# Performance work log

Hardware: AMD Instinct MI355X
Metric: run time of the kernel (lower is better)

Reference implementation:

```python
import jax, jax.numpy as jnp
import numpy as np

D_MODEL = 1024
B, S = 4, 4096


def setup_inputs() -> dict:
    key = jax.random.key(0)
    k1, k2, k3, k4, k5 = jax.random.split(key, 5)
    lim = 1.0 / np.sqrt(D_MODEL)  # nn.Linear default init range
    x = jax.random.normal(k1, (B, S, D_MODEL), dtype=jnp.float32)
    mask = jnp.ones((B, S), dtype=jnp.float32)
    W_up = jax.random.uniform(k2, (D_MODEL, D_MODEL), jnp.float32, -lim, lim)
    b_up = jax.random.uniform(k3, (D_MODEL,), jnp.float32, -lim, lim)
    W_f = jax.random.uniform(k4, (D_MODEL, D_MODEL), jnp.float32, -lim, lim)
    b_f = jax.random.uniform(k5, (D_MODEL,), jnp.float32, -lim, lim)
    decay_param = jnp.zeros((1,), dtype=jnp.float32)
    return {"x": x, "mask": mask, "W_up": W_up, "b_up": b_up,
            "W_f": W_f, "b_f": b_f, "decay_param": decay_param}


def _decay_scan(u, decay):
    # h_t = decay * h_{t-1} + u_t  along axis=1, via associative scan.
    # Element: (a, b) representing h -> a*h + b; compose: (a1*a2, b1*a2 + b2).
    a = jnp.broadcast_to(decay, u.shape)

    def combine(c1, c2):
        a1, b1 = c1
        a2, b2 = c2
        return a1 * a2, b1 * a2 + b2

    _, h = jax.lax.associative_scan(combine, (a, u), axis=1)
    return h


def reference(x, mask, W_up, b_up, W_f, b_f, decay_param):
    decay = jax.nn.sigmoid(decay_param)[0]
    # u_i = mask_i * linear_update(x_i)
    u = (jnp.einsum('bsd,ed->bse', x, W_up) + b_up) * mask[..., None]
    # h_t = sum_{i<=t} decay^(t-i) * u_i  (exponential-decay recurrence)
    h = _decay_scan(u, decay)
    return jnp.einsum('bsd,ed->bse', h, W_f) + b_f
```

## Files before the change

kernel.cpp:

```cpp
#include <hip/hip_runtime.h>
#include <hip/hip_bf16.h>
#include <cstdint>
#include <cstddef>

#define DMODEL 1024
#define BATCH  4
#define SEQ    4096
#define BSROWS (BATCH*SEQ)
#define CHUNK  32
#define NCHUNK (SEQ/CHUNK)
#define NCH_T  (BATCH*NCHUNK)

typedef __attribute__((ext_vector_type(8))) short bf16x8;
typedef __attribute__((ext_vector_type(4))) float f32x4;


__device__ __forceinline__ unsigned short f2bf(float f) {
  union { float f; uint32_t u; } v; v.f = f;
  uint32_t u = v.u;
  u += 0x7FFFu + ((u >> 16) & 1u);
  return (unsigned short)(u >> 16);
}

__device__ __forceinline__ float sigmoid_dev(const float* dp) {
  return 1.0f / (1.0f + expf(-dp[0]));
}

typedef __attribute__((address_space(1))) void void_g;
typedef __attribute__((address_space(3))) void void_l;

__device__ __forceinline__ void gl2lds16(const void* g, void* l) {
  __builtin_amdgcn_global_load_lds((void_g*)g, (void_l*)l, 16, 0, 0);
}

__device__ __forceinline__ void kloop64(
    const unsigned short* __restrict__ A, const unsigned short* __restrict__ B,
    int m0, int n0, f32x4 acc[2][2],
    unsigned short* As, unsigned short* Bs, int tid) {
  int lane = tid & 63, w = tid >> 6, wm = w & 1, wn = w >> 1;
  int quad = lane >> 4, l16 = lane & 15;
  int r = tid >> 3, cch = tid & 7;
  int g = cch ^ (r & 7);

  auto stage = [&](int t, int slot) {
    int k0 = t * 64;
    unsigned short* dA = As + slot * 4096;
    unsigned short* dB = Bs + slot * 4096;
    gl2lds16(A + (size_t)(m0 + r) * DMODEL + k0 + g * 8,      dA + r * 64 + cch * 8);
    gl2lds16(A + (size_t)(m0 + 32 + r) * DMODEL + k0 + g * 8, dA + (32 + r) * 64 + cch * 8);
    gl2lds16(B + (size_t)(n0 + r) * DMODEL + k0 + g * 8,      dB + r * 64 + cch * 8);
    gl2lds16(B + (size_t)(n0 + 32 + r) * DMODEL + k0 + g * 8, dB + (32 + r) * 64 + cch * 8);
  };
  auto compute = [&](int slot) {
    const bf16x8* Av = (const bf16x8*)(As + slot * 4096);
    const bf16x8* Bv = (const bf16x8*)(Bs + slot * 4096);
    #pragma unroll
    for (int kk = 0; kk < 2; ++kk) {
      bf16x8 af[2], bfr[2];
      #pragma unroll
      for (int i = 0; i < 2; ++i) {
        int rowA = wm * 32 + i * 16 + l16;
        af[i]  = Av[rowA * 8 + ((kk * 4 + quad) ^ (l16 & 7))];
        int rowB = wn * 32 + i * 16 + l16;
        bfr[i] = Bv[rowB * 8 + ((kk * 4 + quad) ^ (l16 & 7))];
      }
      __builtin_amdgcn_s_setprio(1);
      #pragma unroll
      for (int i = 0; i < 2; ++i)
        #pragma unroll
        for (int j = 0; j < 2; ++j)
          acc[i][j] = __builtin_amdgcn_mfma_f32_16x16x32_bf16(af[i], bfr[j], acc[i][j], 0, 0, 0);
      __builtin_amdgcn_s_setprio(0);
    }
  };

  stage(0, 0); stage(1, 1);
  asm volatile("s_waitcnt vmcnt(4)" ::: "memory");
  __builtin_amdgcn_s_barrier();
  asm volatile("" ::: "memory");
  int cur = 0;
  for (int t = 0; t < 14; ++t) {
    int ns = cur + 2; if (ns >= 3) ns -= 3;
    stage(t + 2, ns);
    compute(cur);
    asm volatile("s_waitcnt vmcnt(4)" ::: "memory");
    __builtin_amdgcn_s_barrier();
    asm volatile("" ::: "memory");
    cur = (cur == 2) ? 0 : cur + 1;
  }
  compute(cur);
  asm volatile("s_waitcnt vmcnt(0)" ::: "memory");
  __builtin_amdgcn_s_barrier();
  asm volatile("" ::: "memory");
  cur = (cur == 2) ? 0 : cur + 1;
  compute(cur);
}

__global__ __launch_bounds__(256) void prep_kernel(
    const float* __restrict__ x, const float* __restrict__ mask,
    const float* __restrict__ W_up, const float* __restrict__ b_up,
    const float* __restrict__ W_f, const float* __restrict__ dp,
    unsigned short* __restrict__ Wf_bf, unsigned short* __restrict__ WupT,
    float* __restrict__ bb, unsigned short* __restrict__ hv,
    float* __restrict__ carry, float* __restrict__ lbeta,
    float* __restrict__ cbeta) {
  __shared__ float tile[32][33];
  int blk = blockIdx.x;
  int tid = threadIdx.x;

  if (blk < 512) {
    float decay = sigmoid_dev(dp);
    int b = blk / NCHUNK, c = blk % NCHUNK;
    int base = b * SEQ + c * CHUNK;
    const float4* xp = (const float4*)(x + (size_t)base * DMODEL);
    const float4* mp4 = (const float4*)(mask + base);
    float mreg[32];
    #pragma unroll
    for (int q = 0; q < 8; ++q) {
      float4 t = mp4[q];
      mreg[q * 4 + 0] = t.x; mreg[q * 4 + 1] = t.y;
      mreg[q * 4 + 2] = t.z; mreg[q * 4 + 3] = t.w;
    }
    float4 h = make_float4(0.f, 0.f, 0.f, 0.f);
    #pragma unroll
    for (int s = 0; s < CHUNK; ++s) {
      float m = mreg[s];
      float4 xv = xp[(size_t)s * (DMODEL / 4) + tid];
      h.x = decay * h.x + m * xv.x;
      h.y = decay * h.y + m * xv.y;
      h.z = decay * h.z + m * xv.z;
      h.w = decay * h.w + m * xv.w;
      ushort4 o;
      o.x = f2bf(h.x); o.y = f2bf(h.y); o.z = f2bf(h.z); o.w = f2bf(h.w);
      ((ushort4*)hv)[(size_t)(base + s) * (DMODEL / 4) + tid] = o;
    }
    ((float4*)carry)[(size_t)blk * (DMODEL / 4) + tid] = h;
  } else if (blk < 1536) {
    int e = blk - 512;
    int lane = tid & 63, w = tid >> 6;
    float4 v = ((const float4*)(W_f + (size_t)e * DMODEL))[tid];
    float4 bu = ((const float4*)b_up)[tid];
    ushort4 o;
    o.x = f2bf(v.x); o.y = f2bf(v.y); o.z = f2bf(v.z); o.w = f2bf(v.w);
    ((ushort4*)(Wf_bf + (size_t)e * DMODEL))[tid] = o;
    float s = v.x * bu.x + v.y * bu.y + v.z * bu.z + v.w * bu.w;
    #pragma unroll
    for (int off = 32; off; off >>= 1) s += __shfl_down(s, off);
    if (lane == 0) ((float*)tile)[w] = s;
    __syncthreads();
    if (tid == 0)
      bb[e] = ((float*)tile)[0] + ((float*)tile)[1] +
              ((float*)tile)[2] + ((float*)tile)[3];
  } else if (blk < 2560) {
    int id = blk - 1536;
    int bx = id & 31, by = id >> 5;
    int tx = tid & 31, ty = tid >> 5;
    int xx = bx * 32 + tx;
    int y0 = by * 32;
    for (int j = ty; j < 32; j += 8)
      tile[j][tx] = W_up[(size_t)(y0 + j) * DMODEL + xx];
    __syncthreads();
    int dd = tid >> 3;
    int c4 = (tid & 7) * 4;
    ushort4 o;
    o.x = f2bf(tile[c4 + 0][dd]);
    o.y = f2bf(tile[c4 + 1][dd]);
    o.z = f2bf(tile[c4 + 2][dd]);
    o.w = f2bf(tile[c4 + 3][dd]);
    *(ushort4*)(WupT + (size_t)(bx * 32 + dd) * DMODEL + y0 + c4) = o;
  } else {
    float decay = sigmoid_dev(dp);
    int t = (blk - 2560) * 256 + tid;
    int s = t & 31;
    float h = mask[t];
    float wgt = decay;
    #pragma unroll
    for (int off = 1; off < 32; off <<= 1) {
      float up = __shfl_up(h, off);
      if (s >= off) h += wgt * up;
      wgt = wgt * wgt;
    }
    lbeta[t] = h;
    if (s == 31) cbeta[t >> 5] = h;
  }
}

__global__ __launch_bounds__(256) void mid2_kernel(
    const unsigned short* __restrict__ Wf_bf,
    const unsigned short* __restrict__ WupT,
    unsigned short* __restrict__ Wc,
    const float* __restrict__ carry, const float* __restrict__ cbeta,
    const float* __restrict__ dp,
    unsigned short* __restrict__ Pbf, float* __restrict__ pbeta) {
  __shared__ unsigned short As[3 * 64 * 64];
  __shared__ unsigned short Bs[3 * 64 * 64];
  int tid = threadIdx.x;
  if (blockIdx.x < 256) {
    int mt = blockIdx.x >> 4, nt = blockIdx.x & 15;
    f32x4 acc[2][2] = {};
    kloop64(Wf_bf, WupT, mt * 64, nt * 64, acc, As, Bs, tid);
    int lane = tid & 63, w = tid >> 6, wm = w & 1, wn = w >> 1;
    int quad = lane >> 4, l16 = lane & 15;
    #pragma unroll
    for (int j = 0; j < 2; ++j) {
      int col = nt * 64 + wn * 32 + j * 16 + l16;
      #pragma unroll
      for (int i = 0; i < 2; ++i) {
        int rowb = mt * 64 + wm * 32 + i * 16 + quad * 4;
        #pragma unroll
        for (int rr = 0; rr < 4; ++rr)
          Wc[(size_t)(rowb + rr) * DMODEL + col] = f2bf(acc[i][j][rr]);
      }
    }
  } else {
    float decay = sigmoid_dev(dp);
    float dL = powf(decay, (float)CHUNK);
    int gid = (blockIdx.x - 256) * 256 + tid;
    int b = gid >> 10, dd = gid & 1023;
    float P = 0.f;
    for (int c0 = 0; c0 < NCHUNK; c0 += 8) {
      float v[8];
      #pragma unroll
      for (int j = 0; j < 8; ++j)
        v[j] = carry[(size_t)(b * NCHUNK + c0 + j) * DMODEL + dd];
      #pragma unroll
      for (int j = 0; j < 8; ++j) {
        Pbf[(size_t)(b * NCHUNK + c0 + j) * DMODEL + dd] = f2bf(P);
        P = dL * P + v[j];
      }
    }
    if (dd == 0) {
      float Pb = 0.f;
      for (int c0 = 0; c0 < NCHUNK; c0 += 16) {
        float v[16];
        #pragma unroll
        for (int j = 0; j < 16; ++j) v[j] = cbeta[b * NCHUNK + c0 + j];
        #pragma unroll
        for (int j = 0; j < 16; ++j) {
          pbeta[b * NCHUNK + c0 + j] = Pb;
          Pb = dL * Pb + v[j];
        }
      }
    }
  }
}

__global__ __launch_bounds__(256) void pout_kernel(
    const unsigned short* __restrict__ Pbf,
    const unsigned short* __restrict__ Wc,
    const float* __restrict__ pbeta, const float* __restrict__ bb,
    float* __restrict__ Pout) {
  __shared__ unsigned short As[3 * 64 * 64];
  __shared__ unsigned short Bs[3 * 64 * 64];
  int tid = threadIdx.x;
  int mt = blockIdx.x >> 4, nt = blockIdx.x & 15;
  f32x4 acc[2][2] = {};
  kloop64(Pbf, Wc, mt * 64, nt * 64, acc, As, Bs, tid);
  int lane = tid & 63, w = tid >> 6, wm = w & 1, wn = w >> 1;
  int quad = lane >> 4, l16 = lane & 15;
  #pragma unroll
  for (int j = 0; j < 2; ++j) {
    int col = nt * 64 + wn * 32 + j * 16 + l16;
    float bbv = bb[col];
    #pragma unroll
    for (int i = 0; i < 2; ++i) {
      int rowb = mt * 64 + wm * 32 + i * 16 + quad * 4;
      #pragma unroll
      for (int rr = 0; rr < 4; ++rr) {
        int row = rowb + rr;
        Pout[(size_t)row * DMODEL + col] = acc[i][j][rr] + pbeta[row] * bbv;
      }
    }
  }
}

__global__ __launch_bounds__(512) void gemm_main(
    const unsigned short* __restrict__ A,
    const unsigned short* __restrict__ Bm,
    const float* __restrict__ Pout,
    const float* __restrict__ lbeta,
    const float* __restrict__ bb,
    const float* __restrict__ bias_f,
    const float* __restrict__ dp,
    float* __restrict__ out) {
  __shared__ unsigned short As[4 * 256 * 32];
  __shared__ unsigned short Bs[4 * 256 * 32];
  __shared__ float dpow[CHUNK];
  const int SLOT = 256 * 32;
  int tid = threadIdx.x;
  if (tid < CHUNK) {
    float decay = sigmoid_dev(dp);
    dpow[tid] = powf(decay, (float)(tid + 1));
  }
  __syncthreads();

  int lane = tid & 63, wid = tid >> 6;
  int wm = wid >> 2, wn = wid & 3;
  int quad = lane >> 4, l16 = lane & 15;
  int phi = (l16 >> 1) & 3;
  int r = tid >> 2, c4 = tid & 3;
  int g = c4 ^ ((r >> 1) & 3);

  int bid = blockIdx.x;
  int xcd = bid & 7, jb = bid >> 3;
  int m0 = (xcd * 8 + (jb >> 2)) * 256;
  int n0 = (jb & 3) * 256;

  f32x4 acc[8][4] = {};
  bf16x8 bfr[4];

  auto stageA = [&](int t, int slot) {
    int k0 = t * 32;
    unsigned short* dA = As + slot * SLOT;
    gl2lds16(A + (size_t)(m0 + r) * DMODEL + k0 + g * 8,        dA + r * 32 + c4 * 8);
    gl2lds16(A + (size_t)(m0 + 128 + r) * DMODEL + k0 + g * 8,  dA + (128 + r) * 32 + c4 * 8);
  };
  auto stageB = [&](int t, int slot) {
    int k0 = t * 32;
    unsigned short* dB = Bs + slot * SLOT;
    gl2lds16(Bm + (size_t)(n0 + r) * DMODEL + k0 + g * 8,       dB + r * 32 + c4 * 8);
    gl2lds16(Bm + (size_t)(n0 + 128 + r) * DMODEL + k0 + g * 8, dB + (128 + r) * 32 + c4 * 8);
  };
  auto readA = [&](const bf16x8* Av, int mh, bf16x8 af[4]) {
    #pragma unroll
    for (int i = 0; i < 4; ++i) {
      int rowA = wm * 128 + mh * 64 + i * 16 + l16;
      af[i] = Av[rowA * 4 + (quad ^ phi)];
    }
  };
  auto readB = [&](const bf16x8* Bv) {
    #pragma unroll
    for (int j = 0; j < 4; ++j) {
      int rowB = wn * 64 + j * 16 + l16;
      bfr[j] = Bv[rowB * 4 + (quad ^ phi)];
    }
  };
  auto mfma16 = [&](int mh, const bf16x8 af[4]) {
    __builtin_amdgcn_s_setprio(1);
    #pragma unroll
    for (int i = 0; i < 4; ++i)
      #pragma unroll
      for (int j = 0; j < 4; ++j)
        acc[mh * 4 + i][j] =
            __builtin_amdgcn_mfma_f32_16x16x32_bf16(af[i], bfr[j], acc[mh * 4 + i][j], 0, 0, 0);
    __builtin_amdgcn_s_setprio(0);
  };

  stageA(0, 0); stageB(0, 0);
  stageA(1, 1); stageB(1, 1);
  stageA(2, 2); stageB(2, 2);
  asm volatile("s_waitcnt vmcnt(8)" ::: "memory");
  __builtin_amdgcn_s_barrier();
  asm volatile("" ::: "memory");

  for (int t = 0; t < 29; ++t) {
    int cs = t & 3, ss = (t + 3) & 3;
    const bf16x8* Av = (const bf16x8*)(As + cs * SLOT);
    const bf16x8* Bv = (const bf16x8*)(Bs + cs * SLOT);
    bf16x8 af[4];
    readA(Av, 0, af);
    readB(Bv);
    stageA(t + 3, ss);
    __builtin_amdgcn_s_barrier();
    asm volatile("s_waitcnt lgkmcnt(0)" ::: "memory");
    __builtin_amdgcn_sched_barrier(0);
    mfma16(0, af);
    __builtin_amdgcn_s_barrier();
    bf16x8 af2[4];
    readA(Av, 1, af2);
    stageB(t + 3, ss);
    asm volatile("s_waitcnt vmcnt(8)" ::: "memory");
    __builtin_amdgcn_s_barrier();
    asm volatile("s_waitcnt lgkmcnt(0)" ::: "memory");
    __builtin_amdgcn_sched_barrier(0);
    mfma16(1, af2);
    __builtin_amdgcn_s_barrier();
    asm volatile("" ::: "memory");
  }
  auto tailfull = [&](int slot) {
    const bf16x8* Av = (const bf16x8*)(As + slot * SLOT);
    const bf16x8* Bv = (const bf16x8*)(Bs + slot * SLOT);
    bf16x8 af[4];
    readA(Av, 0, af);
    readB(Bv);
    mfma16(0, af);
    readA(Av, 1, af);
    mfma16(1, af);
  };
  tailfull(1);
  asm volatile("s_waitcnt vmcnt(4)" ::: "memory");
  __builtin_amdgcn_s_barrier();
  asm volatile("" ::: "memory");
  tailfull(2);
  asm volatile("s_waitcnt vmcnt(0)" ::: "memory");
  __builtin_amdgcn_s_barrier();
  asm volatile("" ::: "memory");
  tailfull(3);

  float bbv[4], bfv[4];
  #pragma unroll
  for (int j = 0; j < 4; ++j) {
    int col = n0 + wn * 64 + j * 16 + l16;
    bbv[j] = bb[col];
    bfv[j] = bias_f[col];
  }
  #pragma unroll
  for (int i = 0; i < 8; ++i) {
    #pragma unroll
    for (int rr = 0; rr < 4; ++rr) {
      int row = m0 + wm * 128 + i * 16 + quad * 4 + rr;
      float lb  = lbeta[row];
      float dpw = dpow[row & 31];
      const float* poRow = Pout + (size_t)(row >> 5) * DMODEL;
      float* outRow = out + (size_t)row * DMODEL;
      #pragma unroll
      for (int j = 0; j < 4; ++j) {
        int col = n0 + wn * 64 + j * 16 + l16;
        outRow[col] = acc[i][j][rr] + dpw * poRow[col] + lb * bbv[j] + bfv[j];
      }
    }
  }
}


extern "C" void kernel_launch(void* const* d_in, const int* in_sizes, int n_in,
                              void* d_out, int out_size, void* d_ws, size_t ws_size,
                              hipStream_t stream) {
  const float* x    = (const float*)d_in[0];
  const float* mask = (const float*)d_in[1];
  const float* W_up = (const float*)d_in[2];
  const float* b_up = (const float*)d_in[3];
  const float* W_f  = (const float*)d_in[4];
  const float* b_f  = (const float*)d_in[5];
  const float* dp   = (const float*)d_in[6];
  float* out = (float*)d_out;

  char* ws = (char*)d_ws;
  unsigned short* hv    = (unsigned short*)(ws);
  unsigned short* Wc    = (unsigned short*)(ws + 33554432);
  unsigned short* Wf_bf = (unsigned short*)(ws + 35651584);
  unsigned short* WupT  = (unsigned short*)(ws + 37748736);
  float* carry  = (float*)(ws + 39845888);
  unsigned short* Pbf = (unsigned short*)(ws + 41943040);
  float* Pout   = (float*)(ws + 42991616);
  float* lbeta  = (float*)(ws + 45088768);
  float* cbeta  = (float*)(ws + 45154304);
  float* pbeta  = (float*)(ws + 45156352);
  float* bb     = (float*)(ws + 45158400);

  prep_kernel<<<2624, 256, 0, stream>>>(x, mask, W_up, b_up, W_f, dp,
                                        Wf_bf, WupT, bb, hv, carry, lbeta, cbeta);
  mid2_kernel<<<272, 256, 0, stream>>>(Wf_bf, WupT, Wc, carry, cbeta, dp,
                                       Pbf, pbeta);
  pout_kernel<<<128, 256, 0, stream>>>(Pbf, Wc, pbeta, bb, Pout);
  gemm_main<<<256, 512, 0, stream>>>(hv, Wc, Pout, lbeta, bb, b_f, dp, out);
}
```

Measured before the change: 193.9 us.

## Switch main GEMM to double-buffered K=64 tiles with simpler pipeline

```diff
diff --git a/kernel.cpp b/kernel.cpp
--- a/kernel.cpp
+++ b/kernel.cpp
@@ -283,23 +283,21 @@
     const float* __restrict__ bias_f,
     const float* __restrict__ dp,
     float* __restrict__ out) {
-  __shared__ unsigned short As[4 * 256 * 32];
-  __shared__ unsigned short Bs[4 * 256 * 32];
+  __shared__ unsigned short As[2 * 256 * 64];
+  __shared__ unsigned short Bs[2 * 256 * 64];
   __shared__ float dpow[CHUNK];
-  const int SLOT = 256 * 32;
+  const int TSLOT = 256 * 64;
   int tid = threadIdx.x;
   if (tid < CHUNK) {
     float decay = sigmoid_dev(dp);
     dpow[tid] = powf(decay, (float)(tid + 1));
   }
-  __syncthreads();
 
   int lane = tid & 63, wid = tid >> 6;
   int wm = wid >> 2, wn = wid & 3;
   int quad = lane >> 4, l16 = lane & 15;
-  int phi = (l16 >> 1) & 3;
-  int r = tid >> 2, c4 = tid & 3;
-  int g = c4 ^ ((r >> 1) & 3);
+  int r = tid >> 3, cch = tid & 7;
+  int g = cch ^ (r & 7);
 
   int bid = blockIdx.x;
   int xcd = bid & 7, jb = bid >> 3;
@@ -307,95 +305,56 @@
   int n0 = (jb & 3) * 256;
 
   f32x4 acc[8][4] = {};
-  bf16x8 bfr[4];
-
-  auto stageA = [&](int t, int slot) {
-    int k0 = t * 32;
-    unsigned short* dA = As + slot * SLOT;
-    gl2lds16(A + (size_t)(m0 + r) * DMODEL + k0 + g * 8,        dA + r * 32 + c4 * 8);
-    gl2lds16(A + (size_t)(m0 + 128 + r) * DMODEL + k0 + g * 8,  dA + (128 + r) * 32 + c4 * 8);
+
+  auto stageT = [&](int t, int p) {
+    int k0 = t * 64;
+    unsigned short* dA = As + p * TSLOT;
+    unsigned short* dB = Bs + p * TSLOT;
+    #pragma unroll
+    for (int q = 0; q < 4; ++q)
+      gl2lds16(A + (size_t)(m0 + q * 64 + r) * DMODEL + k0 + g * 8,
+               dA + (q * 64 + r) * 64 + cch * 8);
+    #pragma unroll
+    for (int q = 0; q < 4; ++q)
+      gl2lds16(Bm + (size_t)(n0 + q * 64 + r) * DMODEL + k0 + g * 8,
+               dB + (q * 64 + r) * 64 + cch * 8);
   };
-  auto stageB = [&](int t, int slot) {
-    int k0 = t * 32;
-    unsigned short* dB = Bs + slot * SLOT;
-    gl2lds16(Bm + (size_t)(n0 + r) * DMODEL + k0 + g * 8,       dB + r * 32 + c4 * 8);
-    gl2lds16(Bm + (size_t)(n0 + 128 + r) * DMODEL + k0 + g * 8, dB + (128 + r) * 32 + c4 * 8);
+  auto compute = [&](int p) {
+    const bf16x8* Av = (const bf16x8*)(As + p * TSLOT);
+    const bf16x8* Bv = (const bf16x8*)(Bs + p * TSLOT);
+    #pragma unroll
+    for (int kk = 0; kk < 2; ++kk) {
+      bf16x8 bfr[4];
+      #pragma unroll
+      for (int j = 0; j < 4; ++j) {
+        int rowB = wn * 64 + j * 16 + l16;
+        bfr[j] = Bv[rowB * 8 + ((kk * 4 + quad) ^ (l16 & 7))];
+      }
+      #pragma unroll
+      for (int i = 0; i < 8; ++i) {
+        int rowA = wm * 128 + i * 16 + l16;
+        bf16x8 af = Av[rowA * 8 + ((kk * 4 + quad) ^ (l16 & 7))];
+        __builtin_amdgcn_s_setprio(1);
+        #pragma unroll
+        for (int j = 0; j < 4; ++j)
+          acc[i][j] = __builtin_amdgcn_mfma_f32_16x16x32_bf16(af, bfr[j], acc[i][j], 0, 0, 0);
+        __builtin_amdgcn_s_setprio(0);
+      }
+    }
   };
-  auto readA = [&](const bf16x8* Av, int mh, bf16x8 af[4]) {
-    #pragma unroll
-    for (int i = 0; i < 4; ++i) {
-      int rowA = wm * 128 + mh * 64 + i * 16 + l16;
-      af[i] = Av[rowA * 4 + (quad ^ phi)];
-    }
-  };
-  auto readB = [&](const bf16x8* Bv) {
-    #pragma unroll
-    for (int j = 0; j < 4; ++j) {
-      int rowB = wn * 64 + j * 16 + l16;
-      bfr[j] = Bv[rowB * 4 + (quad ^ phi)];
-    }
-  };
-  auto mfma16 = [&](int mh, const bf16x8 af[4]) {
-    __builtin_amdgcn_s_setprio(1);
-    #pragma unroll
-    for (int i = 0; i < 4; ++i)
-      #pragma unroll
-      for (int j = 0; j < 4; ++j)
-        acc[mh * 4 + i][j] =
-            __builtin_amdgcn_mfma_f32_16x16x32_bf16(af[i], bfr[j], acc[mh * 4 + i][j], 0, 0, 0);
-    __builtin_amdgcn_s_setprio(0);
-  };
-
-  stageA(0, 0); stageB(0, 0);
-  stageA(1, 1); stageB(1, 1);
-  stageA(2, 2); stageB(2, 2);
-  asm volatile("s_waitcnt vmcnt(8)" ::: "memory");
-  __builtin_amdgcn_s_barrier();
-  asm volatile("" ::: "memory");
-
-  for (int t = 0; t < 29; ++t) {
-    int cs = t & 3, ss = (t + 3) & 3;
-    const bf16x8* Av = (const bf16x8*)(As + cs * SLOT);
-    const bf16x8* Bv = (const bf16x8*)(Bs + cs * SLOT);
-    bf16x8 af[4];
-    readA(Av, 0, af);
-    readB(Bv);
-    stageA(t + 3, ss);
-    __builtin_amdgcn_s_barrier();
-    asm volatile("s_waitcnt lgkmcnt(0)" ::: "memory");
-    __builtin_amdgcn_sched_barrier(0);
-    mfma16(0, af);
-    __builtin_amdgcn_s_barrier();
-    bf16x8 af2[4];
-    readA(Av, 1, af2);
-    stageB(t + 3, ss);
-    asm volatile("s_waitcnt vmcnt(8)" ::: "memory");
-    __builtin_amdgcn_s_barrier();
-    asm volatile("s_waitcnt lgkmcnt(0)" ::: "memory");
-    __builtin_amdgcn_sched_barrier(0);
-    mfma16(1, af2);
+
+  stageT(0, 0);
+  __syncthreads();
+
+  for (int t = 0; t < 15; ++t) {
+    int p = t & 1;
+    stageT(t + 1, p ^ 1);
+    compute(p);
+    asm volatile("s_waitcnt vmcnt(0)" ::: "memory");
     __builtin_amdgcn_s_barrier();
     asm volatile("" ::: "memory");
   }
-  auto tailfull = [&](int slot) {
-    const bf16x8* Av = (const bf16x8*)(As + slot * SLOT);
-    const bf16x8* Bv = (const bf16x8*)(Bs + slot * SLOT);
-    bf16x8 af[4];
-    readA(Av, 0, af);
-    readB(Bv);
-    mfma16(0, af);
-    readA(Av, 1, af);
-    mfma16(1, af);
-  };
-  tailfull(1);
-  asm volatile("s_waitcnt vmcnt(4)" ::: "memory");
-  __builtin_amdgcn_s_barrier();
-  asm volatile("" ::: "memory");
-  tailfull(2);
-  asm volatile("s_waitcnt vmcnt(0)" ::: "memory");
-  __builtin_amdgcn_s_barrier();
-  asm volatile("" ::: "memory");
-  tailfull(3);
+  compute(1);
 
   float bbv[4], bfv[4];
   #pragma unroll
```

Measured after the change: 191.0 us. No clear change (-1.5%).
